# Optimization experiments

Hardware: AMD Instinct MI355X
Metric: run time of the kernel (lower is better)

## Reference

```python
import jax, jax.numpy as jnp
import numpy as np

DECAY = 0.8
COMMITMENT = 1.0
EPS = 1e-05


def setup_inputs() -> dict:
    key = jax.random.key(0)
    k1, k2 = jax.random.split(key)
    x = jax.random.normal(k1, (8, 4096, 256), dtype=jnp.float32)
    embed = jax.random.normal(k2, (8192, 256), dtype=jnp.float32)
    cluster_size = jnp.zeros((8192,), dtype=jnp.float32)
    embed_avg = embed  # torch registers embed_avg = embed.clone()
    return {"x": x, "embed": embed, "cluster_size": cluster_size, "embed_avg": embed_avg}


def reference(x, embed, cluster_size, embed_avg):
    # EuclideanCodebook.forward (training mode) + VectorQuantize straight-through.
    K, D = embed.shape
    shape = x.shape
    flatten = x.reshape(-1, D)  # [T, D], T = B*N

    dist = (2.0 * (flatten @ embed.T)
            - jnp.sum(flatten * flatten, axis=-1, keepdims=True)
            - jnp.sum(embed * embed, axis=-1)[None, :])  # [T, K]
    embed_ind = jnp.argmax(dist, axis=-1)  # [T]

    quantize = embed[embed_ind].reshape(shape)  # gather

    # EMA codebook statistics (scatter-add instead of materializing one-hot [T,K])
    bins = jax.ops.segment_sum(jnp.ones_like(embed_ind, dtype=x.dtype), embed_ind, num_segments=K)  # [K]
    embed_sum = jax.ops.segment_sum(flatten, embed_ind, num_segments=K)  # [K, D]

    new_cluster_size = cluster_size * DECAY + (1.0 - DECAY) * bins
    new_embed_avg = embed_avg * DECAY + (1.0 - DECAY) * embed_sum

    total = new_cluster_size.sum()
    smoothed = (new_cluster_size + EPS) / (total + K * EPS) * total  # laplace smoothing
    new_embed = new_embed_avg / smoothed[:, None]

    commit_loss = jnp.mean((jax.lax.stop_gradient(quantize) - x) ** 2) * COMMITMENT
    quantize_st = x + jax.lax.stop_gradient(quantize - x)  # straight-through

    ind_out = embed_ind.reshape(shape[:-1])
    return quantize_st, ind_out, commit_loss, new_embed, new_cluster_size, new_embed_avg
```

## Files before the change

### kernel.cpp

```cpp
#include <hip/hip_runtime.h>

#define DECAYF 0.8f
#define OMDF   0.2f
#define EPSF   1e-5f
#define COMMITF 1.0f
#define MARGINF 0.02f
#define FIXCAP  8192

typedef _Float16 h8v __attribute__((ext_vector_type(8)));
typedef float f4v __attribute__((ext_vector_type(4)));

__device__ inline void gload_lds16(const void* g, void* l) {
  __builtin_amdgcn_global_load_lds(
      (const __attribute__((address_space(1))) unsigned int*)g,
      (__attribute__((address_space(3))) unsigned int*)l, 16, 0, 0);
}

__global__ __launch_bounds__(256) void k_pre(
    const float* __restrict__ embed, char* __restrict__ Ews,
    float* __restrict__ zero_p, int zero_n, float* __restrict__ ee, int K, int D)
{
  const int tid = threadIdx.x;
  const int gid0 = blockIdx.x * 256 + tid;
  const int gstride = gridDim.x * 256;

  for (int i = gid0; i < zero_n; i += gstride) zero_p[i] = 0.0f;

  for (int gid = gid0; gid < K * (D / 8); gid += gstride) {
    int k = gid >> 5;
    int d0 = (gid & 31) * 8;
    const float* ep = embed + (size_t)k * D + d0;
    float4 v0 = *(const float4*)(ep);
    float4 v1 = *(const float4*)(ep + 4);
    float f[8] = {v0.x, v0.y, v0.z, v0.w, v1.x, v1.y, v1.z, v1.w};
    h8v h;
#pragma unroll
    for (int e = 0; e < 8; ++e) h[e] = (_Float16)f[e];
    int tt = k >> 6;
    int c = k & 63;
    int byteoff = c * 512 + ((d0 * 2) ^ ((c & 7) << 4));
    *(h8v*)(Ews + (size_t)tt * 32768 + byteoff) = h;
  }

  {
    int wave = tid >> 6;
    int lane = tid & 63;
    int k = blockIdx.x * 4 + wave;
    if (k < K) {
      const float* e = embed + (size_t)k * D;
      float s = 0.f;
      for (int d = lane * 4; d < D; d += 256) {
        float4 v = *reinterpret_cast<const float4*>(e + d);
        s += v.x * v.x + v.y * v.y + v.z * v.z + v.w * v.w;
      }
      for (int off = 32; off > 0; off >>= 1) s += __shfl_down(s, off);
      if (lane == 0) ee[k] = 0.5f * s;
    }
  }
}

__device__ __forceinline__ void upd2(float s, int code, float& b1, float& b2, int& bi) {
  if (s > b1) { b2 = b1; b1 = s; bi = code; }
  else if (s > b2) { b2 = s; }
}

__device__ __forceinline__ void k_body(
    int TT, int NT, char* lds, const char* Ews, const float* ee,
    int w, int lane, int ch, int l15, int rowbyte0,
    const int (&dbyte)[8],
    const h8v (&xh)[2][8], const h8v (&xl)[2][8],
    f4v (&CUR)[2][2], f4v (&PRV)[2][2],
    float EEP0, float EEP1, float& EEC0, float& EEC1,
    float (&best)[2][4], float (&bst2)[2][4], int (&bidx)[2][4])
{
  const int k0 = TT * 64;
  const char* cb = lds + (TT & 1) * 32768;
  if (TT + 1 < NT) {
    const char* src = Ews + (size_t)(TT + 1) * 32768 + w * 8192 + lane * 16;
    char* dst = lds + ((TT + 1) & 1) * 32768 + w * 8192;
#pragma unroll
    for (int q = 0; q < 8; ++q) gload_lds16(src + q * 1024, dst + q * 1024);
  }
  EEC0 = ee[k0 + ch * 32 + l15];
  EEC1 = ee[k0 + ch * 32 + l15 + 16];
  const int c0p = k0 - 64 + ch * 32 + l15;
  const int c1p = c0p + 16;
#pragma unroll
  for (int rf = 0; rf < 2; ++rf) {
    CUR[rf][0] = (f4v){0.f, 0.f, 0.f, 0.f};
    CUR[rf][1] = (f4v){0.f, 0.f, 0.f, 0.f};
  }
  h8v Bh0[2], Bh1[2];
  {
    const char* p = cb + rowbyte0 + dbyte[0];
    Bh0[0] = *(const h8v*)(p);
    Bh1[0] = *(const h8v*)(p + 8192);
  }
#pragma unroll
  for (int ks = 0; ks < 8; ++ks) {
    const int cs = ks & 1, ns = cs ^ 1;
    if (ks < 7) {
      const char* p = cb + rowbyte0 + dbyte[ks + 1];
      Bh0[ns] = *(const h8v*)(p);
      Bh1[ns] = *(const h8v*)(p + 8192);
    }
    __builtin_amdgcn_s_setprio(1);
    CUR[0][0] = __builtin_amdgcn_mfma_f32_16x16x32_f16(xh[0][ks], Bh0[cs], CUR[0][0], 0, 0, 0);
    CUR[0][1] = __builtin_amdgcn_mfma_f32_16x16x32_f16(xh[0][ks], Bh1[cs], CUR[0][1], 0, 0, 0);
    CUR[1][0] = __builtin_amdgcn_mfma_f32_16x16x32_f16(xh[1][ks], Bh0[cs], CUR[1][0], 0, 0, 0);
    CUR[1][1] = __builtin_amdgcn_mfma_f32_16x16x32_f16(xh[1][ks], Bh1[cs], CUR[1][1], 0, 0, 0);
    CUR[0][0] = __builtin_amdgcn_mfma_f32_16x16x32_f16(xl[0][ks], Bh0[cs], CUR[0][0], 0, 0, 0);
    CUR[0][1] = __builtin_amdgcn_mfma_f32_16x16x32_f16(xl[0][ks], Bh1[cs], CUR[0][1], 0, 0, 0);
    CUR[1][0] = __builtin_amdgcn_mfma_f32_16x16x32_f16(xl[1][ks], Bh0[cs], CUR[1][0], 0, 0, 0);
    CUR[1][1] = __builtin_amdgcn_mfma_f32_16x16x32_f16(xl[1][ks], Bh1[cs], CUR[1][1], 0, 0, 0);
    __builtin_amdgcn_s_setprio(0);
    {
      const int rf = ks >> 2, ii = ks & 3;
      upd2(PRV[rf][0][ii] - EEP0, c0p, best[rf][ii], bst2[rf][ii], bidx[rf][ii]);
      upd2(PRV[rf][1][ii] - EEP1, c1p, best[rf][ii], bst2[rf][ii], bidx[rf][ii]);
    }
  }
  __syncthreads();
}

__global__ __launch_bounds__(256, 2) void k_dist(
    const float* __restrict__ x, const char* __restrict__ Ews,
    const float* __restrict__ ee, float* __restrict__ ind_f,
    int* __restrict__ idx_out, int* __restrict__ wl, int* __restrict__ cnt,
    int T, int K)
{
  extern __shared__ char lds[];
  const int tid = threadIdx.x;
  const int w = tid >> 6, lane = tid & 63;
  const int l15 = lane & 15, lk = lane >> 4;
  const int rgrp = w >> 1, ch = w & 1;
  const int row0 = blockIdx.x * 64 + rgrp * 32;
  const int NT = K / 64;

  h8v xh[2][8], xl[2][8];
#pragma unroll
  for (int rf = 0; rf < 2; ++rf) {
    const float* xp = x + (size_t)(row0 + rf * 16 + l15) * 256 + lk * 8;
#pragma unroll
    for (int ks = 0; ks < 8; ++ks) {
      float4 v0 = *(const float4*)(xp + ks * 32);
      float4 v1 = *(const float4*)(xp + ks * 32 + 4);
      float f[8] = {v0.x, v0.y, v0.z, v0.w, v1.x, v1.y, v1.z, v1.w};
      h8v h, l;
#pragma unroll
      for (int e = 0; e < 8; ++e) {
        _Float16 hv = (_Float16)f[e];
        h[e] = hv;
        l[e] = (_Float16)(f[e] - (float)hv);
      }
      xh[rf][ks] = h;
      xl[rf][ks] = l;
    }
  }

  float best[2][4], bst2[2][4];
  int bidx[2][4];
#pragma unroll
  for (int rf = 0; rf < 2; ++rf)
#pragma unroll
    for (int i = 0; i < 4; ++i) { best[rf][i] = -3.0e38f; bst2[rf][i] = -3.0e38f; bidx[rf][i] = 0; }

  const int swz = (l15 & 7) << 4;
  const int rowbyte0 = (ch * 32 + l15) * 512;
  int dbyte[8];
#pragma unroll
  for (int ks = 0; ks < 8; ++ks) dbyte[ks] = (ks * 64 + lk * 16) ^ swz;

  {
    const char* src = Ews + (size_t)w * 8192 + lane * 16;
    char* dst = lds + w * 8192;
#pragma unroll
    for (int q = 0; q < 8; ++q)
      gload_lds16(src + q * 1024, dst + q * 1024);
  }
  __syncthreads();

  f4v accA[2][2], accB[2][2];
#pragma unroll
  for (int rf = 0; rf < 2; ++rf) {
    accB[rf][0] = (f4v){-3.0e38f, -3.0e38f, -3.0e38f, -3.0e38f};
    accB[rf][1] = (f4v){-3.0e38f, -3.0e38f, -3.0e38f, -3.0e38f};
  }
  float eeX0 = 0.f, eeX1 = 0.f, eeY0 = 0.f, eeY1 = 0.f;

  for (int tt = 0; tt < NT; tt += 2) {
    k_body(tt,     NT, lds, Ews, ee, w, lane, ch, l15, rowbyte0, dbyte, xh, xl,
           accA, accB, eeX0, eeX1, eeY0, eeY1, best, bst2, bidx);
    k_body(tt + 1, NT, lds, Ews, ee, w, lane, ch, l15, rowbyte0, dbyte, xh, xl,
           accB, accA, eeY0, eeY1, eeX0, eeX1, best, bst2, bidx);
  }
  {
    const int c0 = (NT - 1) * 64 + ch * 32 + l15, c1 = c0 + 16;
#pragma unroll
    for (int rf = 0; rf < 2; ++rf)
#pragma unroll
      for (int ii = 0; ii < 4; ++ii) {
        upd2(accB[rf][0][ii] - eeX0, c0, best[rf][ii], bst2[rf][ii], bidx[rf][ii]);
        upd2(accB[rf][1][ii] - eeX1, c1, best[rf][ii], bst2[rf][ii], bidx[rf][ii]);
      }
  }

#pragma unroll
  for (int rf = 0; rf < 2; ++rf)
#pragma unroll
    for (int i = 0; i < 4; ++i) {
      float s = best[rf][i], s2 = bst2[rf][i];
      int mi = bidx[rf][i];
#pragma unroll
      for (int off = 1; off < 16; off <<= 1) {
        float os = __shfl_xor(s, off);
        float os2 = __shfl_xor(s2, off);
        int oi = __shfl_xor(mi, off);
        if (os > s || (os == s && oi < mi)) {
          s2 = fmaxf(s, os2);
          s = os; mi = oi;
        } else {
          s2 = fmaxf(s2, os);
        }
      }
      best[rf][i] = s; bst2[rf][i] = s2; bidx[rf][i] = mi;
    }

  float* S  = (float*)lds;
  float* S2 = S + 128;
  int*   MI = (int*)(S2 + 128);
  if (l15 == 0) {
#pragma unroll
    for (int rf = 0; rf < 2; ++rf)
#pragma unroll
      for (int i = 0; i < 4; ++i) {
        int rl = rf * 16 + lk * 4 + i;
        int a = rgrp * 64 + ch * 32 + rl;
        S[a]  = best[rf][i];
        S2[a] = bst2[rf][i];
        MI[a] = bidx[rf][i];
      }
  }
  __syncthreads();
  if (ch == 0 && lane < 32) {
    int a0 = rgrp * 64 + lane;
    float sA = S[a0],      s2A = S2[a0];      int miA = MI[a0];
    float sB = S[a0 + 32], s2B = S2[a0 + 32]; int miB = MI[a0 + 32];
    float s, s2; int mi;
    if (sB > sA || (sB == sA && miB < miA)) { s = sB; mi = miB; s2 = fmaxf(sA, s2B); }
    else                                    { s = sA; mi = miA; s2 = fmaxf(s2A, sB); }
    int row = row0 + lane;
    idx_out[row] = mi;
    ind_f[row] = (float)mi;
    if (s - s2 < MARGINF) {
      int slot = atomicAdd(cnt, 1);
      if (slot < FIXCAP) wl[slot] = row;
    }
  }
}

__global__ __launch_bounds__(256) void k_fix1(
    const float* __restrict__ x, const float* __restrict__ embed,
    const float* __restrict__ ee, const int* __restrict__ wl,
    const int* __restrict__ cnt, float* __restrict__ pval,
    int* __restrict__ pidx)
{
  __shared__ float Xs[8][256];
  const int b = blockIdx.x & 255;
  const int g = blockIdx.x >> 8;
  const int t = threadIdx.x;
  int n = *cnt; if (n > FIXCAP) n = FIXCAP;
  const int c = b * 32 + (t & 31);
  const float* er = embed + (size_t)c * 256;
  const float eec = ee[c];
  const int rl = t >> 5;

  for (int r0 = g * 8; r0 < n; r0 += 32) {
    __syncthreads();
    for (int i = t; i < 8 * 64; i += 256) {
      int rr = i >> 6, dq = i & 63;
      int wi = r0 + rr; if (wi >= n) wi = n - 1;
      int row = wl[wi];
      ((float4*)Xs[rr])[dq] = *(const float4*)(x + (size_t)row * 256 + dq * 4);
    }
    __syncthreads();
    const float* xr = Xs[rl];
    float s0 = 0.f, s1 = 0.f, s2a = 0.f, s3 = 0.f;
#pragma unroll
    for (int d = 0; d < 256; d += 16) {
      float4 e0 = *(const float4*)(er + d);
      float4 e1 = *(const float4*)(er + d + 4);
      float4 e2 = *(const float4*)(er + d + 8);
      float4 e3 = *(const float4*)(er + d + 12);
      s0 = fmaf(xr[d + 0], e0.x, s0);  s0 = fmaf(xr[d + 1], e0.y, s0);
      s0 = fmaf(xr[d + 2], e0.z, s0);  s0 = fmaf(xr[d + 3], e0.w, s0);
      s1 = fmaf(xr[d + 4], e1.x, s1);  s1 = fmaf(xr[d + 5], e1.y, s1);
      s1 = fmaf(xr[d + 6], e1.z, s1);  s1 = fmaf(xr[d + 7], e1.w, s1);
      s2a = fmaf(xr[d + 8], e2.x, s2a);  s2a = fmaf(xr[d + 9], e2.y, s2a);
      s2a = fmaf(xr[d + 10], e2.z, s2a); s2a = fmaf(xr[d + 11], e2.w, s2a);
      s3 = fmaf(xr[d + 12], e3.x, s3);  s3 = fmaf(xr[d + 13], e3.y, s3);
      s3 = fmaf(xr[d + 14], e3.z, s3);  s3 = fmaf(xr[d + 15], e3.w, s3);
    }
    float s = ((s0 + s1) + (s2a + s3)) - eec;
    int mi = c;
#pragma unroll
    for (int off = 1; off < 32; off <<= 1) {
      float os = __shfl_xor(s, off);
      int oi = __shfl_xor(mi, off);
      if (os > s || (os == s && oi < mi)) { s = os; mi = oi; }
    }
    int wi = r0 + rl;
    if ((t & 31) == 0 && wi < n) {
      pval[(size_t)wi * 256 + b] = s;
      pidx[(size_t)wi * 256 + b] = mi;
    }
  }
}

__global__ __launch_bounds__(256) void k_fix2(
    const int* __restrict__ wl, const int* __restrict__ cnt,
    const float* __restrict__ pval, const int* __restrict__ pidx,
    float* __restrict__ ind_f, int* __restrict__ idx_out)
{
  __shared__ float bv[256];
  __shared__ int bi[256];
  const int t = threadIdx.x;
  int n = *cnt; if (n > FIXCAP) n = FIXCAP;
  for (int it = blockIdx.x; it < n; it += gridDim.x) {
    __syncthreads();
    bv[t] = pval[(size_t)it * 256 + t];
    bi[t] = pidx[(size_t)it * 256 + t];
    __syncthreads();
    for (int sh = 128; sh > 0; sh >>= 1) {
      if (t < sh) {
        if (bv[t + sh] > bv[t] || (bv[t + sh] == bv[t] && bi[t + sh] < bi[t])) {
          bv[t] = bv[t + sh]; bi[t] = bi[t + sh];
        }
      }
      __syncthreads();
    }
    if (t == 0) {
      int row = wl[it];
      idx_out[row] = bi[0];
      ind_f[row] = (float)bi[0];
    }
  }
}

__global__ void k_gather(const float* __restrict__ x, const float* __restrict__ embed,
                         const int* __restrict__ idx, float* __restrict__ quant,
                         float* __restrict__ bins, float* __restrict__ esum,
                         float* __restrict__ lslots, int T, int D)
{
  int wave = threadIdx.x >> 6;
  int lane = threadIdx.x & 63;
  int row = blockIdx.x * 4 + wave;
  if (row >= T) return;
  int k = idx[row];
  const float* xr = x + (size_t)row * D;
  const float* er = embed + (size_t)k * D;
  float* qr = quant + (size_t)row * D;
  float* esr = esum + (size_t)k * D;
  float lsum = 0.f;
  for (int d = lane * 4; d < D; d += 256) {
    float4 xv = *reinterpret_cast<const float4*>(xr + d);
    float4 ev = *reinterpret_cast<const float4*>(er + d);
    *reinterpret_cast<float4*>(qr + d) = ev;
    float dx = ev.x - xv.x, dy = ev.y - xv.y, dz = ev.z - xv.z, dw = ev.w - xv.w;
    lsum += dx * dx + dy * dy + dz * dz + dw * dw;
    atomicAdd(esr + d + 0, xv.x);
    atomicAdd(esr + d + 1, xv.y);
    atomicAdd(esr + d + 2, xv.z);
    atomicAdd(esr + d + 3, xv.w);
  }
  for (int off = 32; off > 0; off >>= 1) lsum += __shfl_down(lsum, off);
  if (lane == 0) {
    atomicAdd(&bins[k], 1.0f);
    atomicAdd(&lslots[row & 255], lsum);
  }
}

__global__ void k_ema1(const float* __restrict__ cs, const float* __restrict__ bins,
                       float* __restrict__ ncs, float* __restrict__ total_acc, int K)
{
  int k = blockIdx.x * 256 + threadIdx.x;
  float v = 0.f;
  if (k < K) {
    v = cs[k] * DECAYF + OMDF * bins[k];
    ncs[k] = v;
  }
  for (int off = 32; off > 0; off >>= 1) v += __shfl_down(v, off);
  __shared__ float s4[4];
  if ((threadIdx.x & 63) == 0) s4[threadIdx.x >> 6] = v;
  __syncthreads();
  if (threadIdx.x == 0) atomicAdd(total_acc, s4[0] + s4[1] + s4[2] + s4[3]);
}

__global__ void k_ema2(const float* __restrict__ ea, const float* __restrict__ esum,
                       const float* __restrict__ ncs, const float* __restrict__ total_acc,
                       float* __restrict__ ne, float* __restrict__ nea, int K, int D)
{
  int gid = blockIdx.x * 256 + threadIdx.x;
  if (gid >= K * D) return;
  int k = gid / D;
  float total = *total_acc;
  float c = ncs[k];
  float sm = (c + EPSF) / (total + (float)K * EPSF) * total;
  float v = ea[gid] * DECAYF + OMDF * esum[gid];
  nea[gid] = v;
  ne[gid] = v / sm;
}

__global__ void k_loss(const float* __restrict__ lslots, float* __restrict__ out_loss,
                       float scale)
{
  int tid = threadIdx.x;
  float v = lslots[tid];
  for (int off = 32; off > 0; off >>= 1) v += __shfl_down(v, off);
  __shared__ float s4[4];
  if ((tid & 63) == 0) s4[tid >> 6] = v;
  __syncthreads();
  if (tid == 0) out_loss[0] = (s4[0] + s4[1] + s4[2] + s4[3]) * scale;
}

extern "C" void kernel_launch(void* const* d_in, const int* in_sizes, int n_in,
                              void* d_out, int out_size, void* d_ws, size_t ws_size,
                              hipStream_t stream)
{
  const float* x     = (const float*)d_in[0];
  const float* embed = (const float*)d_in[1];
  const float* cs    = (const float*)d_in[2];
  const float* ea    = (const float*)d_in[3];
  const int K = in_sizes[2];
  const int D = in_sizes[1] / K;
  const int T = in_sizes[0] / D;

  float* out   = (float*)d_out;
  float* o_q   = out;
  float* o_ind = out + (size_t)T * D;
  float* o_ls  = o_ind + T;
  float* o_ne  = o_ls + 1;
  float* o_ncs = o_ne + (size_t)K * D;
  float* o_nea = o_ncs + K;

  float* w      = (float*)d_ws;
  float* ee     = w;
  int*   idx    = (int*)(w + K);
  int*   wl     = (int*)(w + K + T);
  float* bins   = w + K + T + FIXCAP;
  float* esum   = bins + K;
  float* lslots = esum + (size_t)K * D;
  float* total  = lslots + 256;
  int*   cnt    = (int*)(total + 1);
  float* pval   = total + 2;
  int*   pidx   = (int*)(pval + (size_t)FIXCAP * 256);
  int zero_n = K + K * D + 256 + 2;
  size_t ews_off = ((size_t)(K + T + FIXCAP + K + (size_t)K * D + 256 + 2
                             + 2 * (size_t)FIXCAP * 256) + 63) & ~(size_t)63;
  char* Ews = (char*)(w + ews_off);

  k_pre<<<2048, 256, 0, stream>>>(embed, Ews, bins, zero_n, ee, K, D);
  k_dist<<<T / 64, 256, 65536, stream>>>(x, Ews, ee, o_ind, idx, wl, cnt, T, K);
  k_fix1<<<1024, 256, 0, stream>>>(x, embed, ee, wl, cnt, pval, pidx);
  k_fix2<<<1024, 256, 0, stream>>>(wl, cnt, pval, pidx, o_ind, idx);
  k_gather<<<(T + 3) / 4, 256, 0, stream>>>(x, embed, idx, o_q, bins, esum, lslots, T, D);
  k_ema1<<<(K + 255) / 256, 256, 0, stream>>>(cs, bins, o_ncs, total, K);
  k_ema2<<<(K * D + 255) / 256, 256, 0, stream>>>(ea, esum, o_ncs, total, o_ne, o_nea, K, D);
  k_loss<<<1, 256, 0, stream>>>(lslots, o_ls, COMMITF / ((float)T * (float)D));
}
```

Baseline: 512.5 us.

## Drop fp16 low-part MFMA pass and replace scatter atomics with per-code row lists

The distance GEMM stops splitting x into high and low fp16 halves and uses only the high half, which halves the MFMA work in the main kernel. The fix-up margin is widened a little to absorb the extra rounding error. Separately, the per-element atomic scatter of x into embed_sum is replaced by a counting pass that builds per-code row lists, plus an overflow path. The EMA kernel then sums its listed rows directly, one wave per code. This removes heavy float atomics, but it relies on the margin-based fix-up still catching every argmax decided by a near tie.

```diff
diff --git a/kernel.cpp b/kernel.cpp
--- a/kernel.cpp
+++ b/kernel.cpp
@@ -4,8 +4,9 @@
 #define OMDF   0.2f
 #define EPSF   1e-5f
 #define COMMITF 1.0f
-#define MARGINF 0.02f
+#define MARGINF 0.024f
 #define FIXCAP  8192
+#define MAXR    64
 
 typedef _Float16 h8v __attribute__((ext_vector_type(8)));
 typedef float f4v __attribute__((ext_vector_type(4)));
@@ -68,7 +69,7 @@
     int TT, int NT, char* lds, const char* Ews, const float* ee,
     int w, int lane, int ch, int l15, int rowbyte0,
     const int (&dbyte)[8],
-    const h8v (&xh)[2][8], const h8v (&xl)[2][8],
+    const h8v (&xh)[2][8],
     f4v (&CUR)[2][2], f4v (&PRV)[2][2],
     float EEP0, float EEP1, float& EEC0, float& EEC1,
     float (&best)[2][4], float (&bst2)[2][4], int (&bidx)[2][4])
@@ -109,10 +110,6 @@
     CUR[0][1] = __builtin_amdgcn_mfma_f32_16x16x32_f16(xh[0][ks], Bh1[cs], CUR[0][1], 0, 0, 0);
     CUR[1][0] = __builtin_amdgcn_mfma_f32_16x16x32_f16(xh[1][ks], Bh0[cs], CUR[1][0], 0, 0, 0);
     CUR[1][1] = __builtin_amdgcn_mfma_f32_16x16x32_f16(xh[1][ks], Bh1[cs], CUR[1][1], 0, 0, 0);
-    CUR[0][0] = __builtin_amdgcn_mfma_f32_16x16x32_f16(xl[0][ks], Bh0[cs], CUR[0][0], 0, 0, 0);
-    CUR[0][1] = __builtin_amdgcn_mfma_f32_16x16x32_f16(xl[0][ks], Bh1[cs], CUR[0][1], 0, 0, 0);
-    CUR[1][0] = __builtin_amdgcn_mfma_f32_16x16x32_f16(xl[1][ks], Bh0[cs], CUR[1][0], 0, 0, 0);
-    CUR[1][1] = __builtin_amdgcn_mfma_f32_16x16x32_f16(xl[1][ks], Bh1[cs], CUR[1][1], 0, 0, 0);
     __builtin_amdgcn_s_setprio(0);
     {
       const int rf = ks >> 2, ii = ks & 3;
@@ -137,7 +134,7 @@
   const int row0 = blockIdx.x * 64 + rgrp * 32;
   const int NT = K / 64;
 
-  h8v xh[2][8], xl[2][8];
+  h8v xh[2][8];
 #pragma unroll
   for (int rf = 0; rf < 2; ++rf) {
     const float* xp = x + (size_t)(row0 + rf * 16 + l15) * 256 + lk * 8;
@@ -146,15 +143,10 @@
       float4 v0 = *(const float4*)(xp + ks * 32);
       float4 v1 = *(const float4*)(xp + ks * 32 + 4);
       float f[8] = {v0.x, v0.y, v0.z, v0.w, v1.x, v1.y, v1.z, v1.w};
-      h8v h, l;
-#pragma unroll
-      for (int e = 0; e < 8; ++e) {
-        _Float16 hv = (_Float16)f[e];
-        h[e] = hv;
-        l[e] = (_Float16)(f[e] - (float)hv);
-      }
+      h8v h;
+#pragma unroll
+      for (int e = 0; e < 8; ++e) h[e] = (_Float16)f[e];
       xh[rf][ks] = h;
-      xl[rf][ks] = l;
     }
   }
 
@@ -189,9 +181,9 @@
   float eeX0 = 0.f, eeX1 = 0.f, eeY0 = 0.f, eeY1 = 0.f;
 
   for (int tt = 0; tt < NT; tt += 2) {
-    k_body(tt,     NT, lds, Ews, ee, w, lane, ch, l15, rowbyte0, dbyte, xh, xl,
+    k_body(tt,     NT, lds, Ews, ee, w, lane, ch, l15, rowbyte0, dbyte, xh,
            accA, accB, eeX0, eeX1, eeY0, eeY1, best, bst2, bidx);
-    k_body(tt + 1, NT, lds, Ews, ee, w, lane, ch, l15, rowbyte0, dbyte, xh, xl,
+    k_body(tt + 1, NT, lds, Ews, ee, w, lane, ch, l15, rowbyte0, dbyte, xh,
            accB, accA, eeY0, eeY1, eeX0, eeX1, best, bst2, bidx);
   }
   {
@@ -347,9 +339,39 @@
   }
 }
 
+__global__ __launch_bounds__(256) void k_cnt(
+    const int* __restrict__ idx, int* __restrict__ cntr, int* __restrict__ rlist,
+    int* __restrict__ olist, int* __restrict__ ocnt, int T)
+{
+  int r = blockIdx.x * 256 + threadIdx.x;
+  if (r >= T) return;
+  int k = idx[r];
+  int slot = atomicAdd(&cntr[k], 1);
+  if (slot < MAXR) rlist[k * MAXR + slot] = r;
+  else { int o = atomicAdd(ocnt, 1); olist[o] = r; }
+}
+
+__global__ __launch_bounds__(256) void k_ovf(
+    const float* __restrict__ x, const int* __restrict__ idx,
+    const int* __restrict__ olist, const int* __restrict__ ocnt,
+    float* __restrict__ ovfsum)
+{
+  int wave = threadIdx.x >> 6, lane = threadIdx.x & 63;
+  int n = *ocnt;
+  for (int i = blockIdx.x * 4 + wave; i < n; i += gridDim.x * 4) {
+    int row = olist[i];
+    int k = idx[row];
+    int d0 = lane * 4;
+    float4 xv = *(const float4*)(x + (size_t)row * 256 + d0);
+    atomicAdd(&ovfsum[(size_t)k * 256 + d0 + 0], xv.x);
+    atomicAdd(&ovfsum[(size_t)k * 256 + d0 + 1], xv.y);
+    atomicAdd(&ovfsum[(size_t)k * 256 + d0 + 2], xv.z);
+    atomicAdd(&ovfsum[(size_t)k * 256 + d0 + 3], xv.w);
+  }
+}
+
 __global__ void k_gather(const float* __restrict__ x, const float* __restrict__ embed,
                          const int* __restrict__ idx, float* __restrict__ quant,
-                         float* __restrict__ bins, float* __restrict__ esum,
                          float* __restrict__ lslots, int T, int D)
 {
   int wave = threadIdx.x >> 6;
@@ -360,7 +382,6 @@
   const float* xr = x + (size_t)row * D;
   const float* er = embed + (size_t)k * D;
   float* qr = quant + (size_t)row * D;
-  float* esr = esum + (size_t)k * D;
   float lsum = 0.f;
   for (int d = lane * 4; d < D; d += 256) {
     float4 xv = *reinterpret_cast<const float4*>(xr + d);
@@ -368,25 +389,18 @@
     *reinterpret_cast<float4*>(qr + d) = ev;
     float dx = ev.x - xv.x, dy = ev.y - xv.y, dz = ev.z - xv.z, dw = ev.w - xv.w;
     lsum += dx * dx + dy * dy + dz * dz + dw * dw;
-    atomicAdd(esr + d + 0, xv.x);
-    atomicAdd(esr + d + 1, xv.y);
-    atomicAdd(esr + d + 2, xv.z);
-    atomicAdd(esr + d + 3, xv.w);
   }
   for (int off = 32; off > 0; off >>= 1) lsum += __shfl_down(lsum, off);
-  if (lane == 0) {
-    atomicAdd(&bins[k], 1.0f);
-    atomicAdd(&lslots[row & 255], lsum);
-  }
-}
-
-__global__ void k_ema1(const float* __restrict__ cs, const float* __restrict__ bins,
+  if (lane == 0) atomicAdd(&lslots[row & 255], lsum);
+}
+
+__global__ void k_ema1(const float* __restrict__ cs, const int* __restrict__ cntr,
                        float* __restrict__ ncs, float* __restrict__ total_acc, int K)
 {
   int k = blockIdx.x * 256 + threadIdx.x;
   float v = 0.f;
   if (k < K) {
-    v = cs[k] * DECAYF + OMDF * bins[k];
+    v = cs[k] * DECAYF + OMDF * (float)cntr[k];
     ncs[k] = v;
   }
   for (int off = 32; off > 0; off >>= 1) v += __shfl_down(v, off);
@@ -396,19 +410,37 @@
   if (threadIdx.x == 0) atomicAdd(total_acc, s4[0] + s4[1] + s4[2] + s4[3]);
 }
 
-__global__ void k_ema2(const float* __restrict__ ea, const float* __restrict__ esum,
-                       const float* __restrict__ ncs, const float* __restrict__ total_acc,
-                       float* __restrict__ ne, float* __restrict__ nea, int K, int D)
-{
-  int gid = blockIdx.x * 256 + threadIdx.x;
-  if (gid >= K * D) return;
-  int k = gid / D;
+__global__ __launch_bounds__(256) void k_ema2(
+    const float* __restrict__ x, const float* __restrict__ ea,
+    const int* __restrict__ cntr, const int* __restrict__ rlist,
+    const float* __restrict__ ovfsum, const float* __restrict__ ncs,
+    const float* __restrict__ total_acc, float* __restrict__ ne,
+    float* __restrict__ nea, int K, int D)
+{
+  int wave = threadIdx.x >> 6, lane = threadIdx.x & 63;
+  int k = blockIdx.x * 4 + wave;
+  if (k >= K) return;
+  int c = cntr[k];
+  int m = c < MAXR ? c : MAXR;
+  int d0 = lane * 4;
+  float4 s = *(const float4*)(ovfsum + (size_t)k * 256 + d0);
+  for (int i = 0; i < m; ++i) {
+    int r = rlist[k * MAXR + i];
+    float4 xv = *(const float4*)(x + (size_t)r * 256 + d0);
+    s.x += xv.x; s.y += xv.y; s.z += xv.z; s.w += xv.w;
+  }
+  float4 eav = *(const float4*)(ea + (size_t)k * 256 + d0);
   float total = *total_acc;
-  float c = ncs[k];
-  float sm = (c + EPSF) / (total + (float)K * EPSF) * total;
-  float v = ea[gid] * DECAYF + OMDF * esum[gid];
-  nea[gid] = v;
-  ne[gid] = v / sm;
+  float csk = ncs[k];
+  float sm = (csk + EPSF) / (total + (float)K * EPSF) * total;
+  float rs = 1.0f / sm;
+  float v0 = eav.x * DECAYF + OMDF * s.x;
+  float v1 = eav.y * DECAYF + OMDF * s.y;
+  float v2 = eav.z * DECAYF + OMDF * s.z;
+  float v3 = eav.w * DECAYF + OMDF * s.w;
+  size_t o = (size_t)k * 256 + d0;
+  nea[o + 0] = v0; nea[o + 1] = v1; nea[o + 2] = v2; nea[o + 3] = v3;
+  ne[o + 0] = v0 * rs; ne[o + 1] = v1 * rs; ne[o + 2] = v2 * rs; ne[o + 3] = v3 * rs;
 }
 
 __global__ void k_loss(const float* __restrict__ lslots, float* __restrict__ out_loss,
@@ -446,25 +478,30 @@
   float* w      = (float*)d_ws;
   float* ee     = w;
   int*   idx    = (int*)(w + K);
-  int*   wl     = (int*)(w + K + T);
-  float* bins   = w + K + T + FIXCAP;
-  float* esum   = bins + K;
-  float* lslots = esum + (size_t)K * D;
+  int*   wl     = idx + T;
+  float* pval   = (float*)(wl + FIXCAP);
+  int*   pidx   = (int*)(pval + (size_t)FIXCAP * 256);
+  int*   rlist  = pidx + (size_t)FIXCAP * 256;
+  int*   olist  = rlist + (size_t)K * MAXR;
+  float* ovfsum = (float*)(olist + T);
+  float* lslots = ovfsum + (size_t)K * D;
   float* total  = lslots + 256;
   int*   cnt    = (int*)(total + 1);
-  float* pval   = total + 2;
-  int*   pidx   = (int*)(pval + (size_t)FIXCAP * 256);
-  int zero_n = K + K * D + 256 + 2;
-  size_t ews_off = ((size_t)(K + T + FIXCAP + K + (size_t)K * D + 256 + 2
-                             + 2 * (size_t)FIXCAP * 256) + 63) & ~(size_t)63;
+  int*   cntr   = cnt + 1;
+  int*   ocnt   = cntr + K;
+  int zero_n = K * D + 256 + 1 + 1 + K + 1;
+  size_t ews_off = (((size_t)(ocnt + 1 - (int*)w)) + 63) & ~(size_t)63;
   char* Ews = (char*)(w + ews_off);
 
-  k_pre<<<2048, 256, 0, stream>>>(embed, Ews, bins, zero_n, ee, K, D);
+  k_pre<<<2048, 256, 0, stream>>>(embed, Ews, ovfsum, zero_n, ee, K, D);
   k_dist<<<T / 64, 256, 65536, stream>>>(x, Ews, ee, o_ind, idx, wl, cnt, T, K);
   k_fix1<<<1024, 256, 0, stream>>>(x, embed, ee, wl, cnt, pval, pidx);
   k_fix2<<<1024, 256, 0, stream>>>(wl, cnt, pval, pidx, o_ind, idx);
-  k_gather<<<(T + 3) / 4, 256, 0, stream>>>(x, embed, idx, o_q, bins, esum, lslots, T, D);
-  k_ema1<<<(K + 255) / 256, 256, 0, stream>>>(cs, bins, o_ncs, total, K);
-  k_ema2<<<(K * D + 255) / 256, 256, 0, stream>>>(ea, esum, o_ncs, total, o_ne, o_nea, K, D);
+  k_cnt<<<(T + 255) / 256, 256, 0, stream>>>(idx, cntr, rlist, olist, ocnt, T);
+  k_ovf<<<128, 256, 0, stream>>>(x, idx, olist, ocnt, ovfsum);
+  k_gather<<<(T + 3) / 4, 256, 0, stream>>>(x, embed, idx, o_q, lslots, T, D);
+  k_ema1<<<(K + 255) / 256, 256, 0, stream>>>(cs, cntr, o_ncs, total, K);
+  k_ema2<<<(K + 3) / 4, 256, 0, stream>>>(x, ea, cntr, rlist, ovfsum, o_ncs, total,
+                                          o_ne, o_nea, K, D);
   k_loss<<<1, 256, 0, stream>>>(lslots, o_ls, COMMITF / ((float)T * (float)D));
 }
```

Measured after the change: 467.0 us. 8.9% less time.
